# Kernel optimization log

Hardware: AMD Instinct MI355X
Metric: run time of the kernel (lower is better)

The kernel has to match this reference:

```python
import math
import jax, jax.numpy as jnp
import numpy as np

NH = 2            # n_hashes
BSZ = 128         # bucket size (q_cluster_size == k_cluster_size)
H, E, M = 8, 64, 128   # num_heads, dim_per_head, nb_features
SOFTMAX_TEMP = 1.0 / math.sqrt(E)


def setup_inputs() -> dict:
    rng = jax.random.key(0)
    ks = jax.random.split(rng, 8)
    B, N = 4, 4096
    D = H * E
    return {
        "query": jax.random.normal(ks[0], (B, N, D), jnp.float32),
        "key": jax.random.normal(ks[1], (B, N, D), jnp.float32),
        "value": jax.random.normal(ks[2], (B, N, D), jnp.float32),
        "proj_W": jax.random.normal(ks[3], (M, E), jnp.float32),          # performer random features
        "lsh_alpha": jax.random.normal(ks[4], (E + 2, NH), jnp.float32),  # E2LSH projections (xbox+ adds 2 dims)
        "lsh_beta": jax.random.uniform(ks[5], (1, NH), jnp.float32),      # uniform(0, r=1)
        "out_W": jax.random.normal(ks[6], (E, D), jnp.float32) / math.sqrt(D),
        "out_b": jnp.zeros((E,), jnp.float32),
    }


def _split_heads(x, B, N):
    # b n (h e) -> (b h) n e
    return x.reshape(B, N, H, E).transpose(0, 2, 1, 3).reshape(B * H, N, E)


def _xboxplus(q, k):
    # asymmetric MIPS->L2 transform (XBOXPLUS)
    qn = jnp.linalg.norm(q, axis=-1, keepdims=True)
    kn = jnp.linalg.norm(k, axis=-1, keepdims=True)
    MQ = jnp.max(qn, axis=-2, keepdims=True)
    MK = jnp.max(kn, axis=-2, keepdims=True)
    ext_q = jnp.sqrt(jnp.maximum(MQ ** 2 + MK ** 2 - qn ** 2, 0.0))
    ext_k = jnp.sqrt(jnp.maximum(MQ ** 2 + MK ** 2 - kn ** 2, 0.0))
    q_t = jnp.concatenate([q, ext_q, jnp.zeros_like(qn)], axis=-1)
    k_t = jnp.concatenate([k, jnp.zeros_like(kn), ext_k], axis=-1)
    return q_t, k_t


def _feature_map(x, W, is_query):
    # performer softmax kernel features with separated log-scale
    xt = x * math.sqrt(SOFTMAX_TEMP)
    proj = jnp.einsum('bte,me->btm', xt, W)
    log_phi = proj - 0.5 * jnp.sum(xt * xt, axis=-1, keepdims=True) - 0.5 * math.log(M)
    if is_query:
        stab = jnp.max(log_phi, axis=-1, keepdims=True)           # per-position
    else:
        stab = jnp.max(log_phi, axis=(-1, -2), keepdims=True)     # per-batch
    stab = jax.lax.stop_gradient(stab)
    return jnp.exp(log_phi - stab), stab


def _sort_to_buckets(x, perm):
    # x: (bh, T, d), perm: (NH, bh, T) -> (NH, bh, nbuckets, BSZ, d)
    g = jnp.take_along_axis(x[None], perm[..., None], axis=2)
    nh, bh, T, d = g.shape
    return g.reshape(nh, bh, T // BSZ, BSZ, d)


def reference(query, key, value, proj_W, lsh_alpha, lsh_beta, out_W, out_b):
    B, N, D = query.shape
    q = _split_heads(query, B, N)
    k = _split_heads(key, B, N)
    v = _split_heads(value, B, N)

    # ---- LSH clustering (torch.no_grad in original) ----
    q_t, k_t = _xboxplus(jax.lax.stop_gradient(q), jax.lax.stop_gradient(k))
    q_hash = (q_t @ lsh_alpha + lsh_beta).transpose(2, 0, 1)   # (NH, bh, N)
    k_hash = (k_t @ lsh_alpha + lsh_beta).transpose(2, 0, 1)
    q_pos = jnp.argsort(q_hash, axis=-1)
    k_pos = jnp.argsort(k_hash, axis=-1)

    # ---- Performer linear-attention branch ----
    q_prime, q_ls = _feature_map(q, proj_W, True)
    k_prime, k_ls = _feature_map(k, proj_W, False)
    prime_log_scale = q_ls + k_ls                               # (bh, N, 1)

    qk1 = jnp.einsum('btm,bm->bt', q_prime, k_prime.sum(axis=1))        # normalization
    kv = jnp.einsum('bsm,bsd->bmd', k_prime, v)
    qkv = jnp.einsum('btm,bmd->btd', q_prime, kv)

    # ---- bucketed exact attention correction ----
    s_q = _sort_to_buckets(q, q_pos)
    s_k = _sort_to_buckets(k, k_pos)
    s_v = _sort_to_buckets(v, k_pos)
    s_qp = _sort_to_buckets(q_prime, q_pos)
    s_kp = _sort_to_buckets(k_prime, k_pos)
    s_pls = _sort_to_buckets(prime_log_scale, q_pos)            # (NH, bh, nb, BSZ, 1)

    inner = jnp.einsum('hbnie,hbnje->hbnij', s_q, s_k) * SOFTMAX_TEMP
    dots_prime = jnp.einsum('hbnim,hbnjm->hbnij', s_qp, s_kp)

    q_rev = jnp.argsort(q_pos, axis=-1)
    if NH > 1:
        k_rev = jnp.argsort(k_pos, axis=-1)
        q_bidx = (q_rev // BSZ).transpose(1, 2, 0)  # (bh, N, NH)
        k_bidx = (k_rev // BSZ).transpose(1, 2, 0)
        s_qb = _sort_to_buckets(q_bidx, q_pos)      # (NH, bh, nb, BSZ, NH)
        s_kb = _sort_to_buckets(k_bidx, k_pos)
        dup = jnp.sum(s_qb[..., :, None, :] == s_kb[..., None, :, :], axis=-1).astype(inner.dtype)
        inner = inner - jnp.log(dup)
        dots_prime = dots_prime / dup

    dots_lse = jnp.maximum(jnp.max(inner, axis=-1, keepdims=True), s_pls)
    dots = jnp.exp(inner - dots_lse) - dots_prime * jnp.exp(s_pls - dots_lse)
    dots_sum = dots.sum(axis=-1, keepdims=True)
    so = jnp.einsum('hbnij,hbnjd->hbnid', dots, s_v)

    def unsort(s_x):
        nh, bh, nb, bsz, d = s_x.shape
        return jnp.take_along_axis(s_x.reshape(nh, bh, nb * bsz, d), q_rev[..., None], axis=2)

    o = unsort(so)
    logits = unsort(dots_lse)          # (NH, bh, N, 1)
    dots_sum_u = unsort(dots_sum)

    norm_ls = jax.nn.logsumexp(logits, axis=0)                  # (bh, N, 1)
    probs = jnp.exp(logits - norm_ls[None])
    out_lsh = jnp.sum(o * probs, axis=0)
    prime_scale = jnp.exp(prime_log_scale - norm_ls)
    out = out_lsh + qkv * prime_scale
    normalization = (dots_sum_u * probs).sum(axis=0) + qk1[..., None] * prime_scale
    out_n = out / jnp.maximum(normalization, 1e-6)

    out_n = out_n.reshape(B, H, N, E).transpose(0, 2, 1, 3).reshape(B, N, H * E)
    return out_n @ out_W.T + out_b
```

## Files before the change

kernel.cpp:

```cpp
#include <hip/hip_runtime.h>
#include <math.h>

#define BH 32
#define NSEQ 4096
#define EDIM 64
#define MDIM 128
#define NHASH 2
#define NBUCK 32
#define BSZC 128
#define BB 4
#define HH 8
#define DD 512
#define NCHUNK 16

static constexpr size_t OFF_SQQ  = 0;
static constexpr size_t SZ_ROWD  = (size_t)BH*NSEQ*8;
static constexpr size_t OFF_SQK  = OFF_SQQ + SZ_ROWD;
static constexpr size_t OFF_QH   = OFF_SQK + SZ_ROWD;
static constexpr size_t SZ_HASH  = (size_t)NHASH*BH*NSEQ*8;
static constexpr size_t OFF_KH   = OFF_QH + SZ_HASH;
static constexpr size_t OFF_MAXQ = OFF_KH + SZ_HASH;
static constexpr size_t OFF_MAXK = OFF_MAXQ + 256;
static constexpr size_t OFF_KLS  = OFF_MAXK + 256;
static constexpr size_t OFF_QPOS = OFF_KLS + 256;
static constexpr size_t SZ_POS   = (size_t)NHASH*BH*NSEQ*4;
static constexpr size_t OFF_KPOS = OFF_QPOS + SZ_POS;
static constexpr size_t OFF_QREV = OFF_KPOS + SZ_POS;
static constexpr size_t OFF_KREV = OFF_QREV + SZ_POS;
static constexpr size_t OFF_QP   = OFF_KREV + SZ_POS;
static constexpr size_t SZ_PRIME = (size_t)BH*NSEQ*MDIM*4;
static constexpr size_t OFF_KP   = OFF_QP + SZ_PRIME;
static constexpr size_t OFF_QLS  = OFF_KP + SZ_PRIME;
static constexpr size_t OFF_KV   = OFF_QLS + (size_t)BH*NSEQ*4;
static constexpr size_t OFF_KSUM = OFF_KV + (size_t)BH*MDIM*EDIM*4;
static constexpr size_t OFF_O    = OFF_KSUM + (size_t)BH*MDIM*4;
static constexpr size_t OFF_LSE  = OFF_O + (size_t)NHASH*BH*NSEQ*EDIM*4;
static constexpr size_t OFF_DSUM = OFF_LSE + (size_t)NHASH*BH*NSEQ*4;
static constexpr size_t OFF_OUTN = OFF_DSUM + (size_t)NHASH*BH*NSEQ*4;
static constexpr size_t OFF_PKV  = OFF_OUTN + (size_t)BB*NSEQ*DD*4;
static constexpr size_t OFF_PKS  = OFF_PKV + (size_t)BH*NCHUNK*MDIM*EDIM*4;
static constexpr size_t OFF_PROJ = OFF_PKV;

#define SQRT_TEMP 0.3535533905932738f
#define HALF_LOG_M 2.4260151319598085f
#define LN2F 0.6931471805599453f

typedef __bf16 bf16_t;
typedef bf16_t bf16x8 __attribute__((ext_vector_type(8)));
typedef bf16_t bf16x4 __attribute__((ext_vector_type(4)));
typedef float  f32x16_t __attribute__((ext_vector_type(16)));
#define Z16 {0.f,0.f,0.f,0.f,0.f,0.f,0.f,0.f,0.f,0.f,0.f,0.f,0.f,0.f,0.f,0.f}

__device__ __forceinline__ unsigned encF(float f){
  unsigned u = __float_as_uint(f);
  return (u & 0x80000000u) ? ~u : (u | 0x80000000u);
}
__device__ __forceinline__ float decF(unsigned e){
  return __uint_as_float((e & 0x80000000u) ? (e ^ 0x80000000u) : ~e);
}

__global__ void k_init(char* __restrict__ ws){
  int idx = blockIdx.x*256 + threadIdx.x;
  if (idx < BH){
    ((unsigned long long*)(ws+OFF_MAXQ))[idx] = 0ull;
    ((unsigned long long*)(ws+OFF_MAXK))[idx] = 0ull;
    ((unsigned*)(ws+OFF_KLS))[idx] = encF(-INFINITY);
  }
}

__global__ __launch_bounds__(256) void k_sumsq(const float* __restrict__ q, const float* __restrict__ k,
                                               const float* __restrict__ alpha, char* __restrict__ ws){
  int p = blockIdx.x*256 + threadIdx.x;
  int bh = p >> 12, t = p & (NSEQ-1);
  int bo = bh >> 3, hh = bh & 7;
  const float* qr = q + ((size_t)bo*NSEQ + t)*DD + hh*EDIM;
  const float* kr = k + ((size_t)bo*NSEQ + t)*DD + hh*EDIM;
  double sq = 0.0, sk = 0.0, a0 = 0.0, a1 = 0.0, c0 = 0.0, c1 = 0.0;
  for (int e = 0; e < EDIM; e++){
    double a = qr[e], b = kr[e];
    double al0 = alpha[e*2+0], al1 = alpha[e*2+1];
    sq = fma(a, a, sq);  sk = fma(b, b, sk);
    a0 = fma(a, al0, a0); a1 = fma(a, al1, a1);
    c0 = fma(b, al0, c0); c1 = fma(b, al1, c1);
  }
  ((double*)(ws+OFF_SQQ))[p] = sq;
  ((double*)(ws+OFF_SQK))[p] = sk;
  double* proj = (double*)(ws+OFF_PROJ);
  proj[p]                       = a0;
  proj[(size_t)BH*NSEQ   + p]   = a1;
  proj[(size_t)BH*NSEQ*2 + p]   = c0;
  proj[(size_t)BH*NSEQ*3 + p]   = c1;
  int lane = threadIdx.x & 63, wid = threadIdx.x >> 6;
  double mq = sq, mk = sk;
  for (int o = 32; o; o >>= 1){ mq = fmax(mq, __shfl_xor(mq, o)); mk = fmax(mk, __shfl_xor(mk, o)); }
  __shared__ double smq[4], smk[4];
  if (!lane){ smq[wid] = mq; smk[wid] = mk; }
  __syncthreads();
  if (!threadIdx.x){
    double a = fmax(fmax(smq[0], smq[1]), fmax(smq[2], smq[3]));
    double b = fmax(fmax(smk[0], smk[1]), fmax(smk[2], smk[3]));
    atomicMax((unsigned long long*)(ws+OFF_MAXQ) + bh, (unsigned long long)__double_as_longlong(a));
    atomicMax((unsigned long long*)(ws+OFF_MAXK) + bh, (unsigned long long)__double_as_longlong(b));
  }
}

__global__ __launch_bounds__(256) void k_hash(const float* __restrict__ alpha, const float* __restrict__ beta,
                                              char* __restrict__ ws){
  int p = blockIdx.x*256 + threadIdx.x;
  int bh = p >> 12;
  double mqk = ((const double*)(ws+OFF_MAXQ))[bh] + ((const double*)(ws+OFF_MAXK))[bh];
  double sq  = ((const double*)(ws+OFF_SQQ))[p];
  double sk  = ((const double*)(ws+OFF_SQK))[p];
  double extq = sqrt(fmax(mqk - sq, 0.0));
  double extk = sqrt(fmax(mqk - sk, 0.0));
  const double* proj = (const double*)(ws+OFF_PROJ);
  double a0 = proj[p];
  double a1 = proj[(size_t)BH*NSEQ   + p];
  double c0 = proj[(size_t)BH*NSEQ*2 + p];
  double c1 = proj[(size_t)BH*NSEQ*3 + p];
  a0 += extq * (double)alpha[64*2+0]; a1 += extq * (double)alpha[64*2+1];
  c0 += extk * (double)alpha[65*2+0]; c1 += extk * (double)alpha[65*2+1];
  double b0 = beta[0], b1 = beta[1];
  double* qh = (double*)(ws+OFF_QH);
  double* kh = (double*)(ws+OFF_KH);
  qh[p] = a0 + b0; qh[(size_t)BH*NSEQ + p] = a1 + b1;
  kh[p] = c0 + b0; kh[(size_t)BH*NSEQ + p] = c1 + b1;
}

__global__ __launch_bounds__(1024) void k_sort(char* __restrict__ ws){
  int row = blockIdx.x;
  bool isK = row >= NHASH*BH;
  int r = isK ? row - NHASH*BH : row;
  const double* hash = (const double*)(ws + (isK ? OFF_KH : OFF_QH)) + (size_t)r*NSEQ;
  int* pos = (int*)(ws + (isK ? OFF_KPOS : OFF_QPOS)) + (size_t)r*NSEQ;
  int* rev = (int*)(ws + (isK ? OFF_KREV : OFF_QREV)) + (size_t)r*NSEQ;
  __shared__ double ks_[NSEQ];
  __shared__ int    is_[NSEQ];
  for (int i = threadIdx.x; i < NSEQ; i += 1024){ ks_[i] = hash[i]; is_[i] = i; }
  __syncthreads();
  for (int k = 2; k <= NSEQ; k <<= 1){
    for (int j = k >> 1; j > 0; j >>= 1){
      for (int i = threadIdx.x; i < NSEQ; i += 1024){
        int ixj = i ^ j;
        if (ixj > i){
          double a = ks_[i], b = ks_[ixj];
          bool up = ((i & k) == 0);
          if ((a > b) == up){
            ks_[i] = b; ks_[ixj] = a;
            int tmp = is_[i]; is_[i] = is_[ixj]; is_[ixj] = tmp;
          }
        }
      }
      __syncthreads();
    }
  }
  for (int i = threadIdx.x; i < NSEQ; i += 1024){ int t = is_[i]; pos[i] = t; rev[t] = i; }
}

__global__ __launch_bounds__(256) void k_featq(const float* __restrict__ query, const float* __restrict__ projW,
                                               char* __restrict__ ws){
  __shared__ float WT[EDIM*MDIM];
  __shared__ float s_q[4][EDIM];
  int tid = threadIdx.x, lane = tid & 63, wid = tid >> 6;
  for (int l = tid; l < EDIM*MDIM; l += 256) WT[l] = projW[(l & 127)*EDIM + (l >> 7)];
  __syncthreads();
  float* qp  = (float*)(ws+OFF_QP);
  float* qls = (float*)(ws+OFF_QLS);
  for (int it = 0; it < 16; it++){
    int p = blockIdx.x*64 + wid*16 + it;
    int bh = p >> 12, t = p & (NSEQ-1), bo = bh >> 3, hh = bh & 7;
    float xv = query[((size_t)bo*NSEQ + t)*DD + hh*EDIM + lane] * SQRT_TEMP;
    s_q[wid][lane] = xv;
    float ss = xv*xv;
    for (int o = 32; o; o >>= 1) ss += __shfl_xor(ss, o);
    float a0 = 0.f, a1 = 0.f;
    for (int e = 0; e < EDIM; e++){
      float qe = s_q[wid][e];
      a0 = fmaf(qe, WT[e*128 + lane], a0);
      a1 = fmaf(qe, WT[e*128 + 64 + lane], a1);
    }
    float c = 0.5f*ss + HALF_LOG_M;
    float lp0 = a0 - c, lp1 = a1 - c;
    float mx = fmaxf(lp0, lp1);
    for (int o = 32; o; o >>= 1) mx = fmaxf(mx, __shfl_xor(mx, o));
    size_t base = (size_t)p*MDIM;
    qp[base + lane]      = expf(lp0 - mx);
    qp[base + 64 + lane] = expf(lp1 - mx);
    if (!lane) qls[p] = mx;
  }
}

__global__ __launch_bounds__(256) void k_featk(const float* __restrict__ key, const float* __restrict__ projW,
                                               char* __restrict__ ws){
  __shared__ float WT[EDIM*MDIM];
  __shared__ float s_q[4][EDIM];
  int tid = threadIdx.x, lane = tid & 63, wid = tid >> 6;
  for (int l = tid; l < EDIM*MDIM; l += 256) WT[l] = projW[(l & 127)*EDIM + (l >> 7)];
  __syncthreads();
  float* kp = (float*)(ws+OFF_KP);
  int bh0 = (blockIdx.x*64) >> 12;
  float bmax = -INFINITY;
  for (int it = 0; it < 16; it++){
    int p = blockIdx.x*64 + wid*16 + it;
    int bh = p >> 12, t = p & (NSEQ-1), bo = bh >> 3, hh = bh & 7;
    float xv = key[((size_t)bo*NSEQ + t)*DD + hh*EDIM + lane] * SQRT_TEMP;
    s_q[wid][lane] = xv;
    float ss = xv*xv;
    for (int o = 32; o; o >>= 1) ss += __shfl_xor(ss, o);
    float a0 = 0.f, a1 = 0.f;
    for (int e = 0; e < EDIM; e++){
      float qe = s_q[wid][e];
      a0 = fmaf(qe, WT[e*128 + lane], a0);
      a1 = fmaf(qe, WT[e*128 + 64 + lane], a1);
    }
    float c = 0.5f*ss + HALF_LOG_M;
    float lp0 = a0 - c, lp1 = a1 - c;
    size_t base = (size_t)p*MDIM;
    kp[base + lane]      = lp0;
    kp[base + 64 + lane] = lp1;
    float mx = fmaxf(lp0, lp1);
    for (int o = 32; o; o >>= 1) mx = fmaxf(mx, __shfl_xor(mx, o));
    bmax = fmaxf(bmax, mx);
  }
  __shared__ float wm[4];
  if (!lane) wm[wid] = bmax;
  __syncthreads();
  if (!tid){
    float m = fmaxf(fmaxf(wm[0], wm[1]), fmaxf(wm[2], wm[3]));
    atomicMax((unsigned*)(ws+OFF_KLS) + bh0, encF(m));
  }
}

__global__ void k_expk(char* __restrict__ ws){
  size_t idx = (size_t)blockIdx.x*256 + threadIdx.x;
  float4* kp = (float4*)(ws+OFF_KP);
  int b = (int)(idx >> 17);
  float stab = decF(((const unsigned*)(ws+OFF_KLS))[b]);
  float4 v = kp[idx];
  v.x = expf(v.x - stab); v.y = expf(v.y - stab);
  v.z = expf(v.z - stab); v.w = expf(v.w - stab);
  kp[idx] = v;
}

__global__ __launch_bounds__(256, 4) void k_kv(const float* __restrict__ value, char* __restrict__ ws){
  int b = blockIdx.x >> 4;
  int chunk = blockIdx.x & 15;
  int bo = b >> 3, hh = b & 7;
  const float* kp = (const float*)(ws+OFF_KP) + (size_t)b*NSEQ*MDIM;
  __shared__ float skp[32][MDIM];
  __shared__ float sv [32][EDIM];
  int tid = threadIdx.x;
  int d = tid & 63, mg = tid >> 6;
  int m0 = mg*32;
  float acc[32];
  #pragma unroll
  for (int i = 0; i < 32; i++) acc[i] = 0.f;
  float ksacc = 0.f;
  #pragma unroll 1
  for (int s0 = chunk*256; s0 < chunk*256 + 256; s0 += 32){
    __syncthreads();
    {
      const float4* src = (const float4*)(kp + (size_t)s0*MDIM);
      #pragma unroll
      for (int l = tid; l < 32*MDIM/4; l += 256) ((float4*)skp)[l] = src[l];
    }
    #pragma unroll
    for (int l = tid; l < 32*EDIM/4; l += 256){
      int r = l >> 4, c4 = (l & 15) << 2;
      *(float4*)&sv[r][c4] = *(const float4*)(value + ((size_t)bo*NSEQ + s0 + r)*DD + hh*EDIM + c4);
    }
    __syncthreads();
    #pragma unroll 1
    for (int ss = 0; ss < 32; ss += 2){
      float vv0 = sv[ss+0][d];
      float vv1 = sv[ss+1][d];
      #pragma unroll
      for (int mq = 0; mq < 8; mq++){
        float4 k0 = *(const float4*)&skp[ss+0][m0 + mq*4];
        float4 k1 = *(const float4*)&skp[ss+1][m0 + mq*4];
        acc[mq*4+0] = fmaf(k0.x, vv0, acc[mq*4+0]);
        acc[mq*4+1] = fmaf(k0.y, vv0, acc[mq*4+1]);
        acc[mq*4+2] = fmaf(k0.z, vv0, acc[mq*4+2]);
        acc[mq*4+3] = fmaf(k0.w, vv0, acc[mq*4+3]);
        acc[mq*4+0] = fmaf(k1.x, vv1, acc[mq*4+0]);
        acc[mq*4+1] = fmaf(k1.y, vv1, acc[mq*4+1]);
        acc[mq*4+2] = fmaf(k1.z, vv1, acc[mq*4+2]);
        acc[mq*4+3] = fmaf(k1.w, vv1, acc[mq*4+3]);
      }
    }
    if (tid < 128){
      #pragma unroll
      for (int ss = 0; ss < 32; ss++) ksacc += skp[ss][tid];
    }
  }
  float* pkv = (float*)(ws+OFF_PKV) + ((size_t)(b*NCHUNK + chunk)*MDIM + m0)*EDIM + d;
  #pragma unroll
  for (int mi = 0; mi < 32; mi++) pkv[mi*EDIM] = acc[mi];
  if (tid < 128)
    ((float*)(ws+OFF_PKS))[(b*NCHUNK + chunk)*MDIM + tid] = ksacc;
}

__global__ __launch_bounds__(256) void k_kvred(char* __restrict__ ws){
  int blk = blockIdx.x;
  if (blk < 1024){
    int idx = blk*256 + threadIdx.x;
    int b = idx >> 13, rem = idx & 8191;
    const float* pkv = (const float*)(ws+OFF_PKV);
    float s = 0.f;
    #pragma unroll
    for (int c = 0; c < NCHUNK; c++) s += pkv[(((size_t)b*NCHUNK + c) << 13) + rem];
    ((float*)(ws+OFF_KV))[idx] = s;
  } else {
    int j = (blk - 1024)*256 + threadIdx.x;
    const float* pks = (const float*)(ws+OFF_PKS);
    int b = j >> 7, m = j & 127;
    float s = 0.f;
    #pragma unroll
    for (int c = 0; c < NCHUNK; c++) s += pks[(b*NCHUNK + c)*MDIM + m];
    ((float*)(ws+OFF_KSUM))[j] = s;
  }
}

__global__ __launch_bounds__(256, 2) void k_bucket(const float* __restrict__ query,
                                                   const float* __restrict__ key,
                                                   const float* __restrict__ value,
                                                   char* __restrict__ ws){
  __shared__ __align__(16) bf16_t s_kT[128*72];
  __shared__ __align__(16) bf16_t s_kp[128*136];
  __shared__ __align__(16) bf16_t s_v [64*136];
  __shared__ int   s_tq[128], s_tk[128], s_qb[128], s_kb[128];
  __shared__ float s_pls[128];

  int blk = blockIdx.x;
  int h = blk >> 10;
  int b = (blk >> 5) & 31;
  int n = blk & 31;
  int tid = threadIdx.x, lane = tid & 63, wid = tid >> 6;
  int col = lane & 31, half = lane >> 5;
  int bo = b >> 3, hh = b & 7;

  const int* kpos  = (const int*)(ws+OFF_KPOS) + ((size_t)h*BH + b)*NSEQ + n*BSZC;
  const int* qpos  = (const int*)(ws+OFF_QPOS) + ((size_t)h*BH + b)*NSEQ + n*BSZC;
  const int* qrev0 = (const int*)(ws+OFF_QREV) + (size_t)b*NSEQ;
  const int* qrev1 = (const int*)(ws+OFF_QREV) + ((size_t)BH + b)*NSEQ;
  const int* krev0 = (const int*)(ws+OFF_KREV) + (size_t)b*NSEQ;
  const int* krev1 = (const int*)(ws+OFF_KREV) + ((size_t)BH + b)*NSEQ;
  const float* qp_g = (const float*)(ws+OFF_QP) + (size_t)b*NSEQ*MDIM;
  const float* kp_g = (const float*)(ws+OFF_KP) + (size_t)b*NSEQ*MDIM;
  const float* qls  = (const float*)(ws+OFF_QLS) + (size_t)b*NSEQ;
  float klsb = decF(((const unsigned*)(ws+OFF_KLS))[b]);

  if (tid < 128){
    int t = qpos[tid];
    s_tq[tid]  = t;
    s_pls[tid] = qls[t] + klsb;
    s_qb[tid]  = (qrev0[t] >> 7) | ((qrev1[t] >> 7) << 16);
  } else {
    int j = tid - 128;
    int t = kpos[j];
    s_tk[j] = t;
    s_kb[j] = (krev0[t] >> 7) | ((krev1[t] >> 7) << 16);
  }
  __syncthreads();

  for (int l = tid; l < 128*16; l += 256){
    int j = l >> 4, e4 = (l & 15) << 2;
    int t = s_tk[j];
    float4 x = *(const float4*)(key + ((size_t)bo*NSEQ + t)*DD + hh*EDIM + e4);
    bf16x4 y = {(bf16_t)x.x, (bf16_t)x.y, (bf16_t)x.z, (bf16_t)x.w};
    *(bf16x4*)&s_kT[j*72 + e4] = y;
  }
  for (int l = tid; l < 128*32; l += 256){
    int j = l >> 5, m4 = (l & 31) << 2;
    int t = s_tk[j];
    float4 x = *(const float4*)(kp_g + (size_t)t*MDIM + m4);
    bf16x4 y = {(bf16_t)x.x, (bf16_t)x.y, (bf16_t)x.z, (bf16_t)x.w};
    *(bf16x4*)&s_kp[j*136 + m4] = y;
  }
  for (int l = tid; l < 128*64; l += 256){
    int j = l >> 6, d = l & 63;
    int t = s_tk[j];
    s_v[d*136 + j] = (bf16_t)value[((size_t)bo*NSEQ + t)*DD + hh*EDIM + d];
  }
  __syncthreads();

  float* o_g   = (float*)(ws+OFF_O)    + ((size_t)h*BH + b)*NSEQ*EDIM;
  float* lse_g = (float*)(ws+OFF_LSE)  + ((size_t)h*BH + b)*NSEQ;
  float* dsm_g = (float*)(ws+OFF_DSUM) + ((size_t)h*BH + b)*NSEQ;

  int mrow = wid*32 + col;
  int tq_m = s_tq[mrow];

  const float* qr = query + ((size_t)bo*NSEQ + tq_m)*DD + hh*EDIM + half*8;
  bf16x8 aq[4];
  #pragma unroll
  for (int kb = 0; kb < 4; kb++){
    float4 x0 = *(const float4*)(qr + kb*16);
    float4 x1 = *(const float4*)(qr + kb*16 + 4);
    bf16x8 a = {(bf16_t)x0.x,(bf16_t)x0.y,(bf16_t)x0.z,(bf16_t)x0.w,
                (bf16_t)x1.x,(bf16_t)x1.y,(bf16_t)x1.z,(bf16_t)x1.w};
    aq[kb] = a;
  }
  f32x16_t ain[4] = {Z16, Z16, Z16, Z16};
  #pragma unroll
  for (int jt = 0; jt < 4; jt++){
    #pragma unroll
    for (int kb = 0; kb < 4; kb++){
      bf16x8 bk = *(const bf16x8*)&s_kT[(jt*32 + col)*72 + kb*16 + half*8];
      ain[jt] = __builtin_amdgcn_mfma_f32_32x32x16_bf16(aq[kb], bk, ain[jt], 0, 0, 0);
    }
  }

  const float* qpr = qp_g + (size_t)tq_m*MDIM + half*8;
  bf16x8 aqp[8];
  #pragma unroll
  for (int kb = 0; kb < 8; kb++){
    float4 x0 = *(const float4*)(qpr + kb*16);
    float4 x1 = *(const float4*)(qpr + kb*16 + 4);
    bf16x8 a = {(bf16_t)x0.x,(bf16_t)x0.y,(bf16_t)x0.z,(bf16_t)x0.w,
                (bf16_t)x1.x,(bf16_t)x1.y,(bf16_t)x1.z,(bf16_t)x1.w};
    aqp[kb] = a;
  }
  f32x16_t apr[4] = {Z16, Z16, Z16, Z16};
  #pragma unroll
  for (int jt = 0; jt < 4; jt++){
    #pragma unroll
    for (int kb = 0; kb < 8; kb++){
      bf16x8 bk = *(const bf16x8*)&s_kp[(jt*32 + col)*136 + kb*16 + half*8];
      apr[jt] = __builtin_amdgcn_mfma_f32_32x32x16_bf16(aqp[kb], bk, apr[jt], 0, 0, 0);
    }
  }
  __syncthreads();

  float pls_r[16]; int qb_r[16];
  #pragma unroll
  for (int i = 0; i < 16; i++){
    int r = wid*32 + (i & 3) + 8*(i >> 2) + 4*half;
    pls_r[i] = s_pls[r];
    qb_r[i]  = s_qb[r];
  }
  float mx[16];
  #pragma unroll
  for (int i = 0; i < 16; i++) mx[i] = -INFINITY;
  #pragma unroll
  for (int jt = 0; jt < 4; jt++){
    int kbp = s_kb[jt*32 + col];
    int kb0 = kbp & 0xffff, kb1 = kbp >> 16;
    #pragma unroll
    for (int i = 0; i < 16; i++){
      int dup2 = ((qb_r[i] & 0xffff) == kb0) & ((qb_r[i] >> 16) == kb1);
      float in = ain[jt][i]*0.125f - (dup2 ? LN2F : 0.0f);
      float dp = dup2 ? apr[jt][i]*0.5f : apr[jt][i];
      ain[jt][i] = in; apr[jt][i] = dp;
      mx[i] = fmaxf(mx[i], in);
    }
  }
  #pragma unroll
  for (int i = 0; i < 16; i++){
    #pragma unroll
    for (int o = 16; o; o >>= 1) mx[i] = fmaxf(mx[i], __shfl_xor(mx[i], o));
  }
  float L[16], eps[16], dsum[16];
  #pragma unroll
  for (int i = 0; i < 16; i++){
    L[i] = fmaxf(mx[i], pls_r[i]);
    eps[i] = expf(pls_r[i] - L[i]);
    dsum[i] = 0.f;
  }
  #pragma unroll
  for (int jt = 0; jt < 4; jt++){
    #pragma unroll
    for (int i = 0; i < 16; i++){
      float d = expf(ain[jt][i] - L[i]) - apr[jt][i]*eps[i];
      dsum[i] += d;
      int r = wid*32 + (i & 3) + 8*(i >> 2) + 4*half;
      s_kp[r*136 + jt*32 + col] = (bf16_t)d;
    }
  }
  #pragma unroll
  for (int i = 0; i < 16; i++){
    #pragma unroll
    for (int o = 16; o; o >>= 1) dsum[i] += __shfl_xor(dsum[i], o);
  }
  __syncthreads();

  f32x16_t ao[2] = {Z16, Z16};
  #pragma unroll
  for (int kb = 0; kb < 8; kb++){
    bf16x8 ad = *(const bf16x8*)&s_kp[mrow*136 + kb*16 + half*8];
    #pragma unroll
    for (int dt = 0; dt < 2; dt++){
      bf16x8 bv = *(const bf16x8*)&s_v[(dt*32 + col)*136 + kb*16 + half*8];
      ao[dt] = __builtin_amdgcn_mfma_f32_32x32x16_bf16(ad, bv, ao[dt], 0, 0, 0);
    }
  }

  #pragma unroll
  for (int i = 0; i < 16; i++){
    int r = wid*32 + (i & 3) + 8*(i >> 2) + 4*half;
    int t = s_tq[r];
    o_g[(size_t)t*EDIM + col]      = ao[0][i];
    o_g[(size_t)t*EDIM + 32 + col] = ao[1][i];
    if (col == 0){ lse_g[t] = L[i]; dsm_g[t] = dsum[i]; }
  }
}

__global__ __launch_bounds__(256) void k_combine(char* __restrict__ ws){
  int b = blockIdx.x >> 6;
  int chunk = blockIdx.x & 63;
  int tid = threadIdx.x, lane = tid & 63, wid = tid >> 6;
  __shared__ float s_kv[MDIM*EDIM];
  __shared__ float s_ks[MDIM];
  __shared__ float s_qp[4][MDIM];
  const float* kv = (const float*)(ws+OFF_KV) + (size_t)b*MDIM*EDIM;
  for (int l = tid; l < MDIM*EDIM; l += 256) s_kv[l] = kv[l];
  if (tid < MDIM) s_ks[tid] = ((const float*)(ws+OFF_KSUM))[b*MDIM + tid];
  __syncthreads();
  const float* qp_g  = (const float*)(ws+OFF_QP) + (size_t)b*NSEQ*MDIM;
  const float* qls   = (const float*)(ws+OFF_QLS) + (size_t)b*NSEQ;
  const float* lse_g = (const float*)(ws+OFF_LSE);
  const float* dsm_g = (const float*)(ws+OFF_DSUM);
  const float* o_g   = (const float*)(ws+OFF_O);
  float* outn = (float*)(ws+OFF_OUTN);
  float klsb = decF(((const unsigned*)(ws+OFF_KLS))[b]);
  int bo = b >> 3, hh = b & 7;
  for (int it = 0; it < 16; it++){
    int t = chunk*64 + wid*16 + it;
    float qp0 = qp_g[(size_t)t*MDIM + lane];
    float qp1 = qp_g[(size_t)t*MDIM + 64 + lane];
    s_qp[wid][lane] = qp0; s_qp[wid][64 + lane] = qp1;
    float qkv = 0.f;
    for (int m = 0; m < 128; m++) qkv = fmaf(s_qp[wid][m], s_kv[m*64 + lane], qkv);
    float qk1 = qp0*s_ks[lane] + qp1*s_ks[64 + lane];
    for (int o = 32; o; o >>= 1) qk1 += __shfl_xor(qk1, o);
    size_t pidx = (size_t)b*NSEQ + t;
    float l0 = lse_g[pidx], l1 = lse_g[(size_t)BH*NSEQ + pidx];
    float mx = fmaxf(l0, l1);
    float nls = mx + logf(expf(l0 - mx) + expf(l1 - mx));
    float p0 = expf(l0 - nls), p1 = expf(l1 - nls);
    float ps = expf(qls[t] + klsb - nls);
    float o0 = o_g[pidx*EDIM + lane];
    float o1 = o_g[((size_t)BH*NSEQ + pidx)*EDIM + lane];
    float ds0 = dsm_g[pidx], ds1 = dsm_g[(size_t)BH*NSEQ + pidx];
    float outv = o0*p0 + o1*p1 + qkv*ps;
    float nrm  = ds0*p0 + ds1*p1 + qk1*ps;
    outn[((size_t)bo*NSEQ + t)*DD + hh*EDIM + lane] = outv / fmaxf(nrm, 1e-6f);
  }
}

__global__ __launch_bounds__(256) void k_final(const float* __restrict__ outW, const float* __restrict__ outB,
                                               const char* __restrict__ ws, float* __restrict__ out){
  __shared__ float WT[DD*65];
  __shared__ float s_x[4][DD];
  int tid = threadIdx.x, lane = tid & 63, wid = tid >> 6;
  for (int l = tid; l < EDIM*DD; l += 256){
    int e = l >> 9, d = l & 511;
    WT[d*65 + e] = outW[l];
  }
  __syncthreads();
  const float* outn = (const float*)(ws+OFF_OUTN);
  for (int it = 0; it < 16; it++){
    int p = blockIdx.x*64 + wid*16 + it;
    const float* x = outn + (size_t)p*DD;
    #pragma unroll
    for (int c = 0; c < 8; c++) s_x[wid][c*64 + lane] = x[c*64 + lane];
    float acc = 0.f;
    for (int d = 0; d < DD; d++) acc = fmaf(s_x[wid][d], WT[d*65 + lane], acc);
    out[(size_t)p*EDIM + lane] = acc + outB[lane];
  }
}

extern "C" void kernel_launch(void* const* d_in, const int* in_sizes, int n_in,
                              void* d_out, int out_size, void* d_ws, size_t ws_size,
                              hipStream_t stream) {
  const float* query = (const float*)d_in[0];
  const float* key   = (const float*)d_in[1];
  const float* value = (const float*)d_in[2];
  const float* projW = (const float*)d_in[3];
  const float* alpha = (const float*)d_in[4];
  const float* beta  = (const float*)d_in[5];
  const float* outW  = (const float*)d_in[6];
  const float* outB  = (const float*)d_in[7];
  char* ws = (char*)d_ws;
  float* out = (float*)d_out;

  k_init <<<1,    256, 0, stream>>>(ws);
  k_sumsq<<<512,  256, 0, stream>>>(query, key, alpha, ws);
  k_hash <<<512,  256, 0, stream>>>(alpha, beta, ws);
  k_sort <<<128, 1024, 0, stream>>>(ws);
  k_featq<<<2048, 256, 0, stream>>>(query, projW, ws);
  k_featk<<<2048, 256, 0, stream>>>(key, projW, ws);
  k_expk <<<16384,256, 0, stream>>>(ws);
  k_kv   <<<512,  256, 0, stream>>>(value, ws);
  k_kvred<<<1040, 256, 0, stream>>>(ws);
  k_bucket<<<2048,256, 0, stream>>>(query, key, value, ws);
  k_combine<<<2048,256,0, stream>>>(ws);
  k_final<<<256,  256, 0, stream>>>(outW, outB, ws, out);
}
```

Baseline: 794.1 us.

## Use register shuffles for bitonic sort and pre-convert gathered operands to bf16

The bitonic sort now does all compare-exchange stages with stride below 64 in registers using wavefront shuffles. Only the larger strides still go through shared memory, which removes many block-wide barriers. Key features and values are also converted to bf16 once, by the exp kernel and a new conversion kernel, so the bucket kernel gathers half as many bytes with wider vector loads. The cost is extra workspace writes and one more kernel launch, and the conversion buffers reuse regions that later stages also write.

New measurement: 746.6 us. 6.0% less time.

```diff
diff --git a/kernel.cpp b/kernel.cpp
--- a/kernel.cpp
+++ b/kernel.cpp
@@ -40,6 +40,8 @@
 static constexpr size_t OFF_PKV  = OFF_OUTN + (size_t)BB*NSEQ*DD*4;
 static constexpr size_t OFF_PKS  = OFF_PKV + (size_t)BH*NCHUNK*MDIM*EDIM*4;
 static constexpr size_t OFF_PROJ = OFF_PKV;
+static constexpr size_t OFF_KPB  = OFF_OUTN;
+static constexpr size_t OFF_VB   = OFF_PKV;
 
 #define SQRT_TEMP 0.3535533905932738f
 #define HALF_LOG_M 2.4260151319598085f
@@ -136,11 +138,37 @@
   int* rev = (int*)(ws + (isK ? OFF_KREV : OFF_QREV)) + (size_t)r*NSEQ;
   __shared__ double ks_[NSEQ];
   __shared__ int    is_[NSEQ];
-  for (int i = threadIdx.x; i < NSEQ; i += 1024){ ks_[i] = hash[i]; is_[i] = i; }
-  __syncthreads();
-  for (int k = 2; k <= NSEQ; k <<= 1){
-    for (int j = k >> 1; j > 0; j >>= 1){
-      for (int i = threadIdx.x; i < NSEQ; i += 1024){
+  int tid = threadIdx.x, lane = tid & 63;
+
+  double key[4]; int idx[4];
+  #pragma unroll
+  for (int m = 0; m < 4; m++){ int i = m*1024 + tid; key[m] = hash[i]; idx[m] = i; }
+
+  #pragma unroll
+  for (int k = 2; k <= 64; k <<= 1){
+    #pragma unroll
+    for (int j = 32; j > 0; j >>= 1){
+      if (j > (k >> 1)) continue;
+      #pragma unroll
+      for (int m = 0; m < 4; m++){
+        int i = m*1024 + tid;
+        bool up = ((i & k) == 0);
+        double pk = __shfl_xor(key[m], j);
+        int    pi = __shfl_xor(idx[m], j);
+        bool isLower = ((lane & j) == 0);
+        double lo = isLower ? key[m] : pk;
+        double hi = isLower ? pk : key[m];
+        if ((lo > hi) == up){ key[m] = pk; idx[m] = pi; }
+      }
+    }
+  }
+  #pragma unroll
+  for (int m = 0; m < 4; m++){ int i = m*1024 + tid; ks_[i] = key[m]; is_[i] = idx[m]; }
+  __syncthreads();
+
+  for (int k = 128; k <= NSEQ; k <<= 1){
+    for (int j = k >> 1; j >= 64; j >>= 1){
+      for (int i = tid; i < NSEQ; i += 1024){
         int ixj = i ^ j;
         if (ixj > i){
           double a = ks_[i], b = ks_[ixj];
@@ -153,8 +181,27 @@
       }
       __syncthreads();
     }
-  }
-  for (int i = threadIdx.x; i < NSEQ; i += 1024){ int t = is_[i]; pos[i] = t; rev[t] = i; }
+    #pragma unroll
+    for (int m = 0; m < 4; m++){ int i = m*1024 + tid; key[m] = ks_[i]; idx[m] = is_[i]; }
+    #pragma unroll
+    for (int j = 32; j > 0; j >>= 1){
+      #pragma unroll
+      for (int m = 0; m < 4; m++){
+        int i = m*1024 + tid;
+        bool up = ((i & k) == 0);
+        double pk = __shfl_xor(key[m], j);
+        int    pi = __shfl_xor(idx[m], j);
+        bool isLower = ((lane & j) == 0);
+        double lo = isLower ? key[m] : pk;
+        double hi = isLower ? pk : key[m];
+        if ((lo > hi) == up){ key[m] = pk; idx[m] = pi; }
+      }
+    }
+    #pragma unroll
+    for (int m = 0; m < 4; m++){ int i = m*1024 + tid; ks_[i] = key[m]; is_[i] = idx[m]; }
+    __syncthreads();
+  }
+  for (int i = tid; i < NSEQ; i += 1024){ int t = is_[i]; pos[i] = t; rev[t] = i; }
 }
 
 __global__ __launch_bounds__(256) void k_featq(const float* __restrict__ query, const float* __restrict__ projW,
@@ -234,12 +281,14 @@
 __global__ void k_expk(char* __restrict__ ws){
   size_t idx = (size_t)blockIdx.x*256 + threadIdx.x;
   float4* kp = (float4*)(ws+OFF_KP);
+  bf16_t* kpb = (bf16_t*)(ws+OFF_KPB);
   int b = (int)(idx >> 17);
   float stab = decF(((const unsigned*)(ws+OFF_KLS))[b]);
   float4 v = kp[idx];
   v.x = expf(v.x - stab); v.y = expf(v.y - stab);
   v.z = expf(v.z - stab); v.w = expf(v.w - stab);
   kp[idx] = v;
+  *(bf16x4*)(kpb + idx*4) = (bf16x4){(bf16_t)v.x,(bf16_t)v.y,(bf16_t)v.z,(bf16_t)v.w};
 }
 
 __global__ __launch_bounds__(256, 4) void k_kv(const float* __restrict__ value, char* __restrict__ ws){
@@ -321,9 +370,20 @@
   }
 }
 
+__global__ __launch_bounds__(256) void k_cvtv(const float* __restrict__ value, char* __restrict__ ws){
+  bf16_t* vb = (bf16_t*)(ws+OFF_VB);
+  size_t idx = (size_t)blockIdx.x*256 + threadIdx.x;
+  int e4 = (int)(idx & 15) << 2;
+  int t  = (int)((idx >> 4) & 4095);
+  int b  = (int)(idx >> 16);
+  int bo = b >> 3, hh = b & 7;
+  float4 x = *(const float4*)(value + ((size_t)bo*NSEQ + t)*DD + hh*EDIM + e4);
+  *(bf16x4*)(vb + ((size_t)b*NSEQ + t)*EDIM + e4) =
+      (bf16x4){(bf16_t)x.x,(bf16_t)x.y,(bf16_t)x.z,(bf16_t)x.w};
+}
+
 __global__ __launch_bounds__(256, 2) void k_bucket(const float* __restrict__ query,
                                                    const float* __restrict__ key,
-                                                   const float* __restrict__ value,
                                                    char* __restrict__ ws){
   __shared__ __align__(16) bf16_t s_kT[128*72];
   __shared__ __align__(16) bf16_t s_kp[128*136];
@@ -346,7 +406,8 @@
   const int* krev0 = (const int*)(ws+OFF_KREV) + (size_t)b*NSEQ;
   const int* krev1 = (const int*)(ws+OFF_KREV) + ((size_t)BH + b)*NSEQ;
   const float* qp_g = (const float*)(ws+OFF_QP) + (size_t)b*NSEQ*MDIM;
-  const float* kp_g = (const float*)(ws+OFF_KP) + (size_t)b*NSEQ*MDIM;
+  const bf16_t* kpb_g = (const bf16_t*)(ws+OFF_KPB) + (size_t)b*NSEQ*MDIM;
+  const bf16_t* vb_g  = (const bf16_t*)(ws+OFF_VB)  + (size_t)b*NSEQ*EDIM;
   const float* qls  = (const float*)(ws+OFF_QLS) + (size_t)b*NSEQ;
   float klsb = decF(((const unsigned*)(ws+OFF_KLS))[b]);
 
@@ -370,17 +431,17 @@
     bf16x4 y = {(bf16_t)x.x, (bf16_t)x.y, (bf16_t)x.z, (bf16_t)x.w};
     *(bf16x4*)&s_kT[j*72 + e4] = y;
   }
-  for (int l = tid; l < 128*32; l += 256){
-    int j = l >> 5, m4 = (l & 31) << 2;
+  for (int l = tid; l < 128*16; l += 256){
+    int j = l >> 4, m8 = (l & 15) << 3;
     int t = s_tk[j];
-    float4 x = *(const float4*)(kp_g + (size_t)t*MDIM + m4);
-    bf16x4 y = {(bf16_t)x.x, (bf16_t)x.y, (bf16_t)x.z, (bf16_t)x.w};
-    *(bf16x4*)&s_kp[j*136 + m4] = y;
-  }
-  for (int l = tid; l < 128*64; l += 256){
-    int j = l >> 6, d = l & 63;
+    *(bf16x8*)&s_kp[j*136 + m8] = *(const bf16x8*)(kpb_g + (size_t)t*MDIM + m8);
+  }
+  for (int l = tid; l < 128*8; l += 256){
+    int j = l >> 3, d8 = (l & 7) << 3;
     int t = s_tk[j];
-    s_v[d*136 + j] = (bf16_t)value[((size_t)bo*NSEQ + t)*DD + hh*EDIM + d];
+    bf16x8 vv = *(const bf16x8*)(vb_g + (size_t)t*EDIM + d8);
+    #pragma unroll
+    for (int i = 0; i < 8; i++) s_v[(d8+i)*136 + j] = vv[i];
   }
   __syncthreads();
 
@@ -593,7 +654,8 @@
   k_expk <<<16384,256, 0, stream>>>(ws);
   k_kv   <<<512,  256, 0, stream>>>(value, ws);
   k_kvred<<<1040, 256, 0, stream>>>(ws);
-  k_bucket<<<2048,256, 0, stream>>>(query, key, value, ws);
+  k_cvtv <<<8192, 256, 0, stream>>>(value, ws);
+  k_bucket<<<2048,256, 0, stream>>>(query, key, ws);
   k_combine<<<2048,256,0, stream>>>(ws);
   k_final<<<256,  256, 0, stream>>>(outW, outB, ws, out);
 }
```
